# Performance work log

Hardware: AMD Instinct MI355X
Metric: run time of the kernel (lower is better)

## Reference

```python
import jax, jax.numpy as jnp
import numpy as np

B, D, H, W, K = 64, 256, 32, 32, 512


def setup_inputs() -> dict:
    key = jax.random.key(0)
    k1, k2 = jax.random.split(key)
    x = jax.random.normal(k1, (B, D, H, W), dtype=jnp.float32)
    # module inits codebook with torch.rand (uniform [0,1)), shape (emb_dim, num_emb)
    weight = jax.random.uniform(k2, (D, K), dtype=jnp.float32)
    return {"x": x, "weight": weight}


def reference(x, weight):
    """VQ-VAE nearest-embedding lookup.

    x: (B, D, H, W), weight: (D, K).
    Returns (quantized (B, D, H, W), argmin (B, H, W)).
    """
    b, d, h, w = x.shape
    n = h * w
    xf = x.reshape(b, d, n)                       # (B, D, N)
    x_sq = jnp.sum(xf * xf, axis=1)               # (B, N)
    e_sq = jnp.sum(weight * weight, axis=0)       # (K,)
    cross = jnp.einsum('bdn,dk->bnk', xf, weight)  # (B, N, K) GEMM
    dist = x_sq[:, :, None] - 2.0 * cross + e_sq[None, None, :]
    argmin = jnp.argmin(dist, axis=-1)            # (B, N)
    quant = jnp.take(weight, argmin, axis=1)      # (D, B, N) gather of code vectors
    quant = jnp.transpose(quant, (1, 0, 2)).reshape(b, d, h, w)
    return quant, argmin.reshape(b, h, w)
```

## Files before the change

kernel.cpp:

```cpp
#include <hip/hip_runtime.h>

#define DIM    256
#define KCODE  512
#define NPOS   1024
#define BATCH  64
#define NPB    64
#define KSTEPS 16
#define EPS    0.01f

using f16x8  = __attribute__((ext_vector_type(8))) _Float16;
using f32x16 = __attribute__((ext_vector_type(16))) float;

#define WS_CNT   0
#define WS_ESQ   64
#define WS_WPK   4096
#define WS_WT    (4096 + 524288)
#define WS_LIST  (4096 + 1048576)

__global__ __launch_bounds__(256) void prep(const float* __restrict__ w,
                                            _Float16* __restrict__ wpk,
                                            float* __restrict__ wT,
                                            float* __restrict__ esq,
                                            int* __restrict__ cnt) {
    __shared__ float ts[32][33];
    __shared__ double sh[8][32];
    const int tid = threadIdx.x;
    const int blk = blockIdx.x;
    if (blk < 128) {
        int gidx = blk * 4 + (tid >> 6);
        int dg = gidx & 1, cg = (gidx >> 1) & 15, t = gidx >> 5;
        int lane = tid & 63, L = lane & 31, h5 = lane >> 5;
        f16x8 out;
#pragma unroll
        for (int j = 0; j < 8; ++j) {
            float v = w[(t * 16 + h5 * 8 + j) * KCODE + cg * 32 + L];
            _Float16 h = (_Float16)v;
            out[j] = dg ? (_Float16)(v - (float)h) : h;
        }
        *(f16x8*)(wpk + (size_t)gidx * 512 + lane * 8) = out;
    } else if (blk < 256) {
        int tt = blk - 128;
        int kt = tt >> 3, dt = tt & 7;
        int c = tid & 31, rl = tid >> 5;
#pragma unroll
        for (int r = 0; r < 4; ++r) {
            int dloc = rl * 4 + r;
            ts[dloc][c] = w[(dt * 32 + dloc) * KCODE + kt * 32 + c];
        }
        __syncthreads();
#pragma unroll
        for (int r = 0; r < 4; ++r) {
            int kloc = rl * 4 + r;
            wT[(size_t)(kt * 32 + kloc) * DIM + dt * 32 + c] = ts[c][kloc];
        }
    } else if (blk < 272) {
        int idx = blk - 256;
        int code = idx * 32 + (tid & 31);
        int sl = tid >> 5;
        double s = 0.0;
        for (int d = sl * 32; d < sl * 32 + 32; ++d) {
            double v = (double)w[d * KCODE + code];
            s = fma(v, v, s);
        }
        sh[sl][tid & 31] = s;
        __syncthreads();
        if (tid < 32) {
            double t = 0.0;
            for (int i = 0; i < 8; ++i) t += sh[i][tid];
            esq[idx * 32 + tid] = (float)t;
        }
    } else {
        if (tid == 0) *cnt = 0;
    }
}

__global__ __launch_bounds__(512, 4) void vq_main(
    const float* __restrict__ x, const _Float16* __restrict__ wpk,
    const float* __restrict__ esq, const float* __restrict__ wT,
    float* __restrict__ quant, float* __restrict__ argm,
    int* __restrict__ cnt, int* __restrict__ list) {

    __shared__ __align__(128) unsigned char smem[67584];
    unsigned char* Bt = smem;
    float* esq_s  = (float*)(smem + 65536);
    float* red1   = (float*)smem;
    float* red2   = (float*)(smem + 2048);
    int*   redi   = (int*)(smem + 4096);
    float* qt     = (float*)(smem + 6144);
    float* bestv  = (float*)(smem + 22784);
    int*   idxbuf = (int*)(smem + 23040);

    const int tid  = threadIdx.x;
    const int wv   = tid >> 6;
    const int lane = tid & 63;
    const int L    = lane & 31;
    const int h5   = lane >> 5;

    const int p0 = blockIdx.x * NPB;
    const int b  = p0 >> 10;
    const int n0 = p0 & (NPOS - 1);

    const int pos = tid & 63;
    const int tg  = tid >> 6;

    esq_s[tid] = esq[tid];

#pragma unroll
    for (int tt = 0; tt < 2; ++tt) {
        int t = tg * 2 + tt;
#pragma unroll
        for (int hh = 0; hh < 2; ++hh) {
            const float* xp = x + ((size_t)b * DIM + t * 16 + hh * 8) * NPOS + n0 + pos;
            f16x8 vh, vl;
#pragma unroll
            for (int j = 0; j < 8; ++j) {
                float v = xp[(size_t)j * NPOS];
                _Float16 h = (_Float16)v;
                vh[j] = h;
                vl[j] = (_Float16)(v - (float)h);
            }
            *(f16x8*)(Bt + ((((t * 2 + hh) * 2) + 0) * NPB + pos) * 16) = vh;
            *(f16x8*)(Bt + ((((t * 2 + hh) * 2) + 1) * NPB + pos) * 16) = vl;
        }
    }
    __syncthreads();

    f32x16 acc[2][2] = {};

#pragma unroll
    for (int t = 0; t < KSTEPS; ++t) {
        f16x8 Ah[2][2];
#pragma unroll
        for (int fm = 0; fm < 2; ++fm)
#pragma unroll
            for (int dg = 0; dg < 2; ++dg)
                Ah[fm][dg] = *(const f16x8*)(
                    wpk + (size_t)(((t * 16 + wv * 2 + fm) * 2 + dg) * 64 + lane) * 8);
        f16x8 Bf[2][2];
#pragma unroll
        for (int fn = 0; fn < 2; ++fn)
#pragma unroll
            for (int dg = 0; dg < 2; ++dg)
                Bf[fn][dg] = *(const f16x8*)(
                    Bt + ((((t * 2 + h5) * 2) + dg) * NPB + fn * 32 + L) * 16);
        __builtin_amdgcn_s_setprio(1);
#pragma unroll
        for (int fm = 0; fm < 2; ++fm)
#pragma unroll
            for (int fn = 0; fn < 2; ++fn) {
                acc[fm][fn] = __builtin_amdgcn_mfma_f32_32x32x16_f16(Ah[fm][0], Bf[fn][0], acc[fm][fn], 0, 0, 0);
                acc[fm][fn] = __builtin_amdgcn_mfma_f32_32x32x16_f16(Ah[fm][1], Bf[fn][0], acc[fm][fn], 0, 0, 0);
                acc[fm][fn] = __builtin_amdgcn_mfma_f32_32x32x16_f16(Ah[fm][0], Bf[fn][1], acc[fm][fn], 0, 0, 0);
            }
        __builtin_amdgcn_s_setprio(0);
    }
    __syncthreads();

    float v1[2] = {3.4e38f, 3.4e38f};
    float v2[2] = {3.4e38f, 3.4e38f};
#pragma unroll
    for (int fm = 0; fm < 2; ++fm)
#pragma unroll
        for (int r = 0; r < 16; ++r) {
            int code = wv * 64 + fm * 32 + (r & 3) + 8 * (r >> 2) + 4 * h5;
            float e = esq_s[code];
#pragma unroll
            for (int fn = 0; fn < 2; ++fn) {
                float s = fmaf(-2.f, acc[fm][fn][r], e);
                acc[fm][fn][r] = s;
                float lo_ = fminf(s, v1[fn]);
                float hi_ = fmaxf(s, v1[fn]);
                v1[fn] = lo_;
                v2[fn] = fminf(v2[fn], hi_);
            }
        }
#pragma unroll
    for (int fn = 0; fn < 2; ++fn) {
        float o1 = __shfl_xor(v1[fn], 32, 64);
        float o2 = __shfl_xor(v2[fn], 32, 64);
        float mn = fminf(v1[fn], o1);
        float mx = fmaxf(v1[fn], o1);
        v1[fn] = mn;
        v2[fn] = fminf(fminf(v2[fn], o2), mx);
        if (h5 == 0) { red1[wv * NPB + fn * 32 + L] = v1[fn]; red2[wv * NPB + fn * 32 + L] = v2[fn]; }
    }
    __syncthreads();
    if (tid < NPB) {
        float g1 = red1[tid], g2 = red2[tid];
#pragma unroll
        for (int wvi = 1; wvi < 8; ++wvi) {
            float a1 = red1[wvi * NPB + tid], a2 = red2[wvi * NPB + tid];
            float mn = fminf(g1, a1), mx = fmaxf(g1, a1);
            g1 = mn; g2 = fminf(fminf(g2, a2), mx);
        }
        bestv[tid] = g1;
        if (g2 - g1 < EPS) {
            int slot = atomicAdd(cnt, 1);
            list[slot] = p0 + tid;
        }
    }
    __syncthreads();
#pragma unroll
    for (int fn = 0; fn < 2; ++fn) {
        float tgt = bestv[fn * 32 + L];
        int cand = 0x7FFFFFFF;
#pragma unroll
        for (int fm = 0; fm < 2; ++fm)
#pragma unroll
            for (int r = 0; r < 16; ++r) {
                int code = wv * 64 + fm * 32 + (r & 3) + 8 * (r >> 2) + 4 * h5;
                if (acc[fm][fn][r] == tgt) cand = min(cand, code);
            }
        int oc = __shfl_xor(cand, 32, 64);
        cand = min(cand, oc);
        if (h5 == 0) redi[wv * NPB + fn * 32 + L] = cand;
    }
    __syncthreads();
    if (tid < NPB) {
        int bi = redi[tid];
#pragma unroll
        for (int wvi = 1; wvi < 8; ++wvi) bi = min(bi, redi[wvi * NPB + tid]);
        idxbuf[tid] = bi;
        argm[(size_t)b * NPOS + n0 + tid] = (float)bi;
    }
    __syncthreads();

    for (int ch = 0; ch < 4; ++ch) {
#pragma unroll
        for (int it = 0; it < 8; ++it) {
            int pp = it * 8 + wv;
            int bi = idxbuf[pp];
            qt[pp * 65 + lane] = wT[(size_t)bi * DIM + ch * 64 + lane];
        }
        __syncthreads();
#pragma unroll
        for (int i = 0; i < 8; ++i) {
            int d = ch * 64 + i * 8 + tg;
            quant[((size_t)b * DIM + d) * NPOS + n0 + pos] = qt[pos * 65 + i * 8 + tg];
        }
        __syncthreads();
    }
}

__global__ __launch_bounds__(512) void refine(const float* __restrict__ x,
                                              const float* __restrict__ w,
                                              float* __restrict__ quant,
                                              float* __restrict__ argm,
                                              const int* __restrict__ cnt,
                                              const int* __restrict__ list) {
    __shared__ float  xs[DIM];
    __shared__ double dv[512];
    __shared__ int    di[512];
    const int tid = threadIdx.x;
    const int n = *cnt;
    for (int i = blockIdx.x; i < n; i += gridDim.x) {
        const int p = list[i];
        const size_t pb = (size_t)(p >> 10), pn = (size_t)(p & (NPOS - 1));
        if (tid < DIM) xs[tid] = x[(pb * DIM + tid) * NPOS + pn];
        __syncthreads();
        double acc = 0.0, sw = 0.0;
#pragma unroll 8
        for (int d = 0; d < DIM; ++d) {
            double wv = (double)w[d * KCODE + tid];
            double xv = (double)xs[d];
            acc = fma(wv, xv, acc);
            sw  = fma(wv, wv, sw);
        }
        dv[tid] = sw - 2.0 * acc;
        di[tid] = tid;
        __syncthreads();
        for (int off = 256; off > 0; off >>= 1) {
            if (tid < off) {
                double ov = dv[tid + off]; int oi = di[tid + off];
                if (ov < dv[tid] || (ov == dv[tid] && oi < di[tid])) { dv[tid] = ov; di[tid] = oi; }
            }
            __syncthreads();
        }
        const int bsel = di[0];
        if (tid == 0) argm[pb * NPOS + pn] = (float)bsel;
        if (tid < DIM) quant[(pb * DIM + tid) * NPOS + pn] = w[tid * KCODE + bsel];
        __syncthreads();
    }
}

extern "C" void kernel_launch(void* const* d_in, const int* in_sizes, int n_in,
                              void* d_out, int out_size, void* d_ws, size_t ws_size,
                              hipStream_t stream) {
    (void)in_sizes; (void)n_in; (void)out_size; (void)ws_size;
    const float* x = (const float*)d_in[0];
    const float* w = (const float*)d_in[1];
    float* quant = (float*)d_out;
    float* argm  = quant + (size_t)BATCH * DIM * NPOS;
    char* ws = (char*)d_ws;
    int*      cnt = (int*)(ws + WS_CNT);
    float*    esq = (float*)(ws + WS_ESQ);
    _Float16* wpk = (_Float16*)(ws + WS_WPK);
    float*    wT  = (float*)(ws + WS_WT);
    int*      list = (int*)(ws + WS_LIST);

    prep<<<273, 256, 0, stream>>>(w, wpk, wT, esq, cnt);
    vq_main<<<(BATCH * NPOS) / NPB, 512, 0, stream>>>(x, wpk, esq, wT, quant, argm, cnt, list);
    refine<<<2048, 512, 0, stream>>>(x, w, quant, argm, cnt, list);
}
```

Before: 98.91 us.

## Interleave MFMA chains across accumulators and stagger K-step order between wave halves

The inner GEMM loop now issues the three split-precision MFMAs round-robin across the four accumulators instead of back-to-back on one accumulator, which removes dependent-MFMA stalls. Waves 4-7 walk the K dimension starting at step 8 while waves 0-3 start at step 0, so the two groups hit different LDS and global regions at the same time and contend less. The s_setprio hints are removed. The summation order changes for half the waves, which can alter fp32 rounding slightly, and the extra branch duplicates the unrolled code.

```diff
diff --git a/kernel.cpp b/kernel.cpp
--- a/kernel.cpp
+++ b/kernel.cpp
@@ -127,32 +127,48 @@
 
     f32x16 acc[2][2] = {};
 
-#pragma unroll
-    for (int t = 0; t < KSTEPS; ++t) {
-        f16x8 Ah[2][2];
-#pragma unroll
-        for (int fm = 0; fm < 2; ++fm)
-#pragma unroll
-            for (int dg = 0; dg < 2; ++dg)
-                Ah[fm][dg] = *(const f16x8*)(
-                    wpk + (size_t)(((t * 16 + wv * 2 + fm) * 2 + dg) * 64 + lane) * 8);
-        f16x8 Bf[2][2];
-#pragma unroll
-        for (int fn = 0; fn < 2; ++fn)
-#pragma unroll
-            for (int dg = 0; dg < 2; ++dg)
-                Bf[fn][dg] = *(const f16x8*)(
-                    Bt + ((((t * 2 + h5) * 2) + dg) * NPB + fn * 32 + L) * 16);
-        __builtin_amdgcn_s_setprio(1);
-#pragma unroll
-        for (int fm = 0; fm < 2; ++fm)
-#pragma unroll
-            for (int fn = 0; fn < 2; ++fn) {
-                acc[fm][fn] = __builtin_amdgcn_mfma_f32_32x32x16_f16(Ah[fm][0], Bf[fn][0], acc[fm][fn], 0, 0, 0);
-                acc[fm][fn] = __builtin_amdgcn_mfma_f32_32x32x16_f16(Ah[fm][1], Bf[fn][0], acc[fm][fn], 0, 0, 0);
-                acc[fm][fn] = __builtin_amdgcn_mfma_f32_32x32x16_f16(Ah[fm][0], Bf[fn][1], acc[fm][fn], 0, 0, 0);
-            }
-        __builtin_amdgcn_s_setprio(0);
+#define STEP(t)                                                                   \
+    {                                                                             \
+        f16x8 Ah[2][2];                                        \
+        _Pragma("unroll")                                                         \
+        for (int fm = 0; fm < 2; ++fm)                                            \
+            _Pragma("unroll")                                                     \
+            for (int dg = 0; dg < 2; ++dg)                                        \
+                Ah[fm][dg] = *(const f16x8*)(                                     \
+                    wpk + (size_t)((((t) * 16 + wv * 2 + fm) * 2 + dg) * 64 + lane) * 8); \
+        f16x8 Bf[2][2];                                        \
+        _Pragma("unroll")                                                         \
+        for (int fn = 0; fn < 2; ++fn)                                            \
+            _Pragma("unroll")                                                     \
+            for (int dg = 0; dg < 2; ++dg)                                        \
+                Bf[fn][dg] = *(const f16x8*)(                                     \
+                    Bt + (((((t) * 2 + h5) * 2) + dg) * NPB + fn * 32 + L) * 16); \
+        _Pragma("unroll")                                                         \
+        for (int fm = 0; fm < 2; ++fm)                                            \
+            _Pragma("unroll")                                                     \
+            for (int fn = 0; fn < 2; ++fn)                                        \
+                acc[fm][fn] = __builtin_amdgcn_mfma_f32_32x32x16_f16(Ah[fm][0], Bf[fn][0], acc[fm][fn], 0, 0, 0); \
+        _Pragma("unroll")                                                         \
+        for (int fm = 0; fm < 2; ++fm)                                            \
+            _Pragma("unroll")                                                     \
+            for (int fn = 0; fn < 2; ++fn)                                        \
+                acc[fm][fn] = __builtin_amdgcn_mfma_f32_32x32x16_f16(Ah[fm][1], Bf[fn][0], acc[fm][fn], 0, 0, 0); \
+        _Pragma("unroll")                                                         \
+        for (int fm = 0; fm < 2; ++fm)                                            \
+            _Pragma("unroll")                                                     \
+            for (int fn = 0; fn < 2; ++fn)                                        \
+                acc[fm][fn] = __builtin_amdgcn_mfma_f32_32x32x16_f16(Ah[fm][0], Bf[fn][1], acc[fm][fn], 0, 0, 0); \
+    }
+
+    if (wv < 4) {
+#pragma unroll
+        for (int t = 0; t < KSTEPS; ++t) STEP(t);
+    } else {
+#pragma unroll
+        for (int tt = 0; tt < KSTEPS; ++tt) {
+            const int t = (tt + 8) & (KSTEPS - 1);
+            STEP(t);
+        }
     }
     __syncthreads();
 
```

Measured after the change: 97.83 us. About the same (-1.1%).
